# Optimization experiments

Hardware: AMD Instinct MI355X
Metric: run time of the kernel (lower is better)

## Reference

```python
import jax, jax.numpy as jnp
import numpy as np
from jax import lax

B, VLEN, H, DIM, C = 32, 2048, 1024, 1024, 32  # batch, value len, hidden_dim, dim, conv_out_channel


def setup_inputs() -> dict:
    key = jax.random.key(0)
    ks = jax.random.split(key, 13)
    s = 0.02
    return {
        "query": jax.random.normal(ks[0], (B, 1, H), dtype=jnp.float32),
        "value": jax.random.normal(ks[1], (B, VLEN, H), dtype=jnp.float32),
        "prev_attn": jax.random.uniform(ks[2], (B, VLEN), dtype=jnp.float32),
        "conv_w": jax.random.normal(ks[3], (C, 1, 3), dtype=jnp.float32) * s,   # Conv1d weight (out,in,k)
        "conv_b": jax.random.normal(ks[4], (C,), dtype=jnp.float32) * s,
        "w_loc": jax.random.normal(ks[5], (DIM, C), dtype=jnp.float32) * s,     # loc_projection (no bias)
        "w_q": jax.random.normal(ks[6], (DIM, H), dtype=jnp.float32) * s,       # query_projection (no bias)
        "w_v": jax.random.normal(ks[7], (DIM, H), dtype=jnp.float32) * s,       # value_projection (no bias)
        "bias": jax.random.uniform(ks[8], (DIM,), dtype=jnp.float32, minval=-0.1, maxval=0.1),
        "w_score": jax.random.normal(ks[9], (1, DIM), dtype=jnp.float32) * s,   # score_projection weight
        "b_score": jax.random.normal(ks[10], (1,), dtype=jnp.float32) * s,
        "w_out": jax.random.normal(ks[11], (H, 2 * H), dtype=jnp.float32) * s,  # out_projection weight
        "b_out": jax.random.normal(ks[12], (H,), dtype=jnp.float32) * s,
    }


def reference(query, value, prev_attn, conv_w, conv_b, w_loc, w_q, w_v, bias,
              w_score, b_score, w_out, b_out):
    # Location features: Conv1d(1 -> C, k=3, pad=1) over prev_attn, then transpose to (B, V, C)
    conv = lax.conv_general_dilated(
        prev_attn[:, None, :], conv_w, window_strides=(1,), padding=[(1, 1)],
        dimension_numbers=("NCH", "OIH", "NCH"),
    ) + conv_b[None, :, None]                       # (B, C, V)
    conv_feat = jnp.transpose(conv, (0, 2, 1))      # (B, V, C)

    qp = jnp.einsum("bqh,dh->bqd", query, w_q)      # (B, 1, DIM)
    vp = jnp.einsum("bvh,dh->bvd", value, w_v)      # (B, V, DIM)
    lp = jnp.einsum("bvc,dc->bvd", conv_feat, w_loc)

    e = jnp.tanh(qp + vp + lp + bias)               # (B, V, DIM), qp broadcasts over V
    score = jnp.einsum("bvd,d->bv", e, w_score[0]) + b_score[0]  # (B, V)

    # smoothing=True: sigmoid then normalize
    s = jax.nn.sigmoid(score)
    attn = s / jnp.sum(s, axis=-1, keepdims=True)   # (B, V)

    context = jnp.einsum("bv,bvh->bh", attn, value)               # (B, H)
    combined = jnp.concatenate([context[:, None, :], query], axis=2)  # (B, 1, 2H)
    output = jnp.einsum("bqk,hk->bqh", combined, w_out) + b_out       # (B, 1, H)
    return output, attn
```

## Files before the change

### kernel.cpp

```cpp
#include <hip/hip_runtime.h>
#include <hip/hip_bf16.h>
#include <math.h>

#define B_SZ 32
#define VLEN_SZ 2048
#define H_SZ 1024
#define DIM_SZ 1024
#define C_SZ 32

typedef float f32x4 __attribute__((ext_vector_type(4)));
typedef short s16x8 __attribute__((ext_vector_type(8)));
typedef short s16x4 __attribute__((ext_vector_type(4)));
typedef unsigned int u32x4 __attribute__((ext_vector_type(4)));

__device__ __forceinline__ short f2bf(float f) {
  unsigned u = __float_as_uint(f);
  u = (u + 0x7fffu + ((u >> 16) & 1u)) >> 16;
  return (short)u;
}

__device__ __forceinline__ float bf2f(short s) {
  return __uint_as_float(((unsigned)(unsigned short)s) << 16);
}

__device__ __forceinline__ unsigned pack2(float a, float b) {
  return __builtin_amdgcn_perm(__float_as_uint(b), __float_as_uint(a), 0x07060302u);
}

__device__ __forceinline__ float fast_tanh(float x) {
  float z = __expf(2.0f * x);
  return 1.0f - 2.0f / (z + 1.0f);
}

__device__ __forceinline__ void ldg_lds16(const void* g, void* l) {
  __builtin_amdgcn_global_load_lds(
      (const __attribute__((address_space(1))) unsigned int*)g,
      (__attribute__((address_space(3))) unsigned int*)l, 16, 0, 0);
}

__global__ __launch_bounds__(256) void k_prep(
    const float* __restrict__ query, const float* __restrict__ w_q,
    const float* __restrict__ bias, const float* __restrict__ prev,
    const float* __restrict__ conv_w, const float* __restrict__ conv_b,
    const float* __restrict__ w_loc, const float* __restrict__ w_v,
    const float* __restrict__ value,
    float* __restrict__ qpb, short* __restrict__ cfb, short* __restrict__ wlocb,
    short* __restrict__ wvb, short* __restrict__ vb,
    float* __restrict__ score, float* __restrict__ context) {
  int bid = blockIdx.x;
  int t = threadIdx.x;
  if (bid < 8192) {
    int wid = bid * 4 + (t >> 6);
    int lane = t & 63;
    int d = wid >> 5;
    int b = wid & 31;
    const f32x4* q4 = (const f32x4*)(query + (size_t)b * H_SZ);
    const f32x4* w4 = (const f32x4*)(w_q + (size_t)d * H_SZ);
    float acc = 0.f;
#pragma unroll
    for (int it = 0; it < 4; ++it) {
      int k = it * 64 + lane;
      f32x4 a = q4[k], w = w4[k];
      acc += a[0] * w[0] + a[1] * w[1] + a[2] * w[2] + a[3] * w[3];
    }
#pragma unroll
    for (int off = 32; off; off >>= 1) acc += __shfl_xor(acc, off, 64);
    if (lane == 0) qpb[(size_t)b * DIM_SZ + d] = acc + bias[d];
  } else if (bid < 8448) {
    int r = (bid - 8192) * 256 + t;
    int v = r & (VLEN_SZ - 1);
    float p0 = prev[r];
    float pm = (v > 0) ? prev[r - 1] : 0.f;
    float pp = (v < VLEN_SZ - 1) ? prev[r + 1] : 0.f;
    float o[C_SZ];
#pragma unroll
    for (int c = 0; c < C_SZ; ++c)
      o[c] = conv_b[c] + pm * conv_w[c * 3 + 0] + p0 * conv_w[c * 3 + 1] + pp * conv_w[c * 3 + 2];
    s16x8* dst = (s16x8*)(cfb + (size_t)r * C_SZ);
#pragma unroll
    for (int g = 0; g < 4; ++g) {
      s16x8 pk;
#pragma unroll
      for (int e = 0; e < 8; ++e) pk[e] = f2bf(o[8 * g + e]);
      dst[g] = pk;
    }
  } else if (bid < 8480) {
    int i = (bid - 8448) * 256 + t;
    f32x4 v = ((const f32x4*)w_loc)[i];
    s16x4 o;
    o[0] = f2bf(v[0]); o[1] = f2bf(v[1]); o[2] = f2bf(v[2]); o[3] = f2bf(v[3]);
    ((s16x4*)wlocb)[i] = o;
  } else if (bid < 9504) {
    int i = (bid - 8480) * 256 + t;
    f32x4 v = ((const f32x4*)w_v)[i];
    s16x4 o;
    o[0] = f2bf(v[0]); o[1] = f2bf(v[1]); o[2] = f2bf(v[2]); o[3] = f2bf(v[3]);
    ((s16x4*)wvb)[i] = o;
  } else if (bid < 9568) {
    int i = (bid - 9504) * 256 + t;
    ((f32x4*)score)[i] = (f32x4){0.f, 0.f, 0.f, 0.f};
  } else if (bid < 9600) {
    int i = (bid - 9568) * 256 + t;
    ((f32x4*)context)[i] = (f32x4){0.f, 0.f, 0.f, 0.f};
  } else {
    size_t i = (size_t)(bid - 9600) * 256 + t;
    const f32x4* src = (const f32x4*)value;
    f32x4 v0 = src[2 * i], v1 = src[2 * i + 1];
    s16x8 o;
    o[0] = f2bf(v0[0]); o[1] = f2bf(v0[1]); o[2] = f2bf(v0[2]); o[3] = f2bf(v0[3]);
    o[4] = f2bf(v1[0]); o[5] = f2bf(v1[1]); o[6] = f2bf(v1[2]); o[7] = f2bf(v1[3]);
    ((s16x8*)vb)[i] = o;
  }
}

#define STAGE_A(ktv, bi_)                                                    \
  do {                                                                       \
    const short* s0_ = ((ktv) < 32) ? aBaseV + (size_t)(ktv) * 32 : aBaseC;  \
    const short* s1_ = ((ktv) < 32) ? aBaseV + (size_t)(ktv) * 32 + 131072   \
                                    : aBaseC + 4096;                         \
    ldg_lds16(s0_, ldw + (bi_) * 16384);                                     \
    ldg_lds16(s1_, ldw + (bi_) * 16384 + 4096);                              \
  } while (0)

#define STAGE_B(ktv, bi_)                                                    \
  do {                                                                       \
    const short* s0_ = ((ktv) < 32) ? bBaseV + (size_t)(ktv) * 32 : bBaseC;  \
    const short* s1_ = ((ktv) < 32) ? bBaseV + (size_t)(ktv) * 32 + 131072   \
                                    : bBaseC + 4096;                         \
    ldg_lds16(s0_, ldw + (bi_) * 16384 + 8192);                              \
    ldg_lds16(s1_, ldw + (bi_) * 16384 + 12288);                             \
  } while (0)

__global__ __launch_bounds__(512, 2) void k_score8(
    const short* __restrict__ vb, const short* __restrict__ wvb,
    const short* __restrict__ wlocb, const short* __restrict__ cfb,
    const float* __restrict__ qpb, const float* __restrict__ w_score,
    float* __restrict__ score) {
  __shared__ short lds_s[3 * 16384];
  __shared__ float sred[8][128];

  int t = threadIdx.x;
  int w = t >> 6, l = t & 63;
  int q = l >> 4, l16 = l & 15;
  int wm = w >> 2, wn = w & 3;
  int bid = blockIdx.x;
  int x = bid & 7, j = bid >> 3;
  int nt = j & 3, mt = x * 32 + (j >> 2);
  int row0 = mt * 256, d0 = nt * 256;
  int b = row0 >> 11;

  int ar = l >> 2;
  int cc = ((l & 3) ^ ((l >> 3) & 3)) * 8;
  int roff = w * 16 + ar;
  const short* aBaseV = vb + (size_t)(row0 + roff) * H_SZ + cc;
  const short* bBaseV = wvb + (size_t)(d0 + roff) * H_SZ + cc;
  const short* aBaseC = cfb + (size_t)(row0 + roff) * C_SZ + cc;
  const short* bBaseC = wlocb + (size_t)(d0 + roff) * C_SZ + cc;
  short* ldw = lds_s + w * 512;

  int posf = (q ^ ((l16 >> 1) & 3)) * 8;

  f32x4 acc[8][4];
#pragma unroll
  for (int i = 0; i < 8; ++i)
#pragma unroll
    for (int n = 0; n < 4; ++n) acc[i][n] = (f32x4){0.f, 0.f, 0.f, 0.f};

  STAGE_A(0, 0); STAGE_B(0, 0);
  STAGE_A(1, 1); STAGE_B(1, 1);
  asm volatile("s_waitcnt vmcnt(4)" ::: "memory");
  __builtin_amdgcn_s_barrier();

  int bi = 0, bs = 2;
  for (int kt = 0; kt < 33; ++kt) {
    const short* As = lds_s + bi * 16384;
    const short* Bs = As + 8192;
    if (kt <= 30) { STAGE_A(kt + 2, bs); STAGE_B(kt + 2, bs); }

    s16x8 af[8], bf[4];
#pragma unroll
    for (int m = 0; m < 8; ++m)
      af[m] = *(const s16x8*)(As + (wm * 128 + m * 16 + l16) * 32 + posf);
#pragma unroll
    for (int n = 0; n < 4; ++n)
      bf[n] = *(const s16x8*)(Bs + (wn * 64 + n * 16 + l16) * 32 + posf);

    __builtin_amdgcn_s_setprio(1);
#pragma unroll
    for (int m = 0; m < 8; ++m)
#pragma unroll
      for (int n = 0; n < 4; ++n)
        acc[m][n] = __builtin_amdgcn_mfma_f32_16x16x32_bf16(af[m], bf[n], acc[m][n], 0, 0, 0);
    __builtin_amdgcn_s_setprio(0);

    if (kt < 31) {
      asm volatile("s_waitcnt vmcnt(4)" ::: "memory");
    } else if (kt == 31) {
      asm volatile("s_waitcnt vmcnt(0)" ::: "memory");
    }
    __builtin_amdgcn_s_barrier();
    bi = (bi == 2) ? 0 : bi + 1;
    bs = (bs == 2) ? 0 : bs + 1;
  }

  float qv[4], wv[4];
#pragma unroll
  for (int n = 0; n < 4; ++n) {
    int d = d0 + wn * 64 + n * 16 + l16;
    qv[n] = qpb[(size_t)b * DIM_SZ + d];
    wv[n] = w_score[d];
  }
#pragma unroll
  for (int i = 0; i < 8; ++i) {
#pragma unroll
    for (int r = 0; r < 4; ++r) {
      float part = 0.f;
#pragma unroll
      for (int n = 0; n < 4; ++n)
        part += fast_tanh(acc[i][n][r] + qv[n]) * wv[n];
      part += __shfl_xor(part, 1);
      part += __shfl_xor(part, 2);
      part += __shfl_xor(part, 4);
      part += __shfl_xor(part, 8);
      if (l16 == 0) sred[w][i * 16 + q * 4 + r] = part;
    }
  }
  __syncthreads();
  if (t < 256) {
    int wmh = t >> 7, lr = t & 127;
    float v = sred[wmh * 4][lr] + sred[wmh * 4 + 1][lr] +
              sred[wmh * 4 + 2][lr] + sred[wmh * 4 + 3][lr];
    atomicAdd(&score[row0 + t], v);
  }
}

__global__ __launch_bounds__(256) void k_prep_f32(
    const float* __restrict__ query, const float* __restrict__ w_q,
    const float* __restrict__ bias, const float* __restrict__ prev,
    const float* __restrict__ conv_w, const float* __restrict__ conv_b,
    const float* __restrict__ w_loc, const float* __restrict__ w_v,
    float* __restrict__ qpb, float* __restrict__ cff, short* __restrict__ wlocb,
    short* __restrict__ wvb, float* __restrict__ score, float* __restrict__ context) {
  int bid = blockIdx.x;
  int t = threadIdx.x;
  if (bid < 8192) {
    int wid = bid * 4 + (t >> 6);
    int lane = t & 63;
    int d = wid >> 5;
    int b = wid & 31;
    const f32x4* q4 = (const f32x4*)(query + (size_t)b * H_SZ);
    const f32x4* w4 = (const f32x4*)(w_q + (size_t)d * H_SZ);
    float acc = 0.f;
#pragma unroll
    for (int it = 0; it < 4; ++it) {
      int k = it * 64 + lane;
      f32x4 a = q4[k], w = w4[k];
      acc += a[0] * w[0] + a[1] * w[1] + a[2] * w[2] + a[3] * w[3];
    }
#pragma unroll
    for (int off = 32; off; off >>= 1) acc += __shfl_xor(acc, off, 64);
    if (lane == 0) qpb[(size_t)b * DIM_SZ + d] = acc + bias[d];
  } else if (bid < 8448) {
    int r = (bid - 8192) * 256 + t;
    int v = r & (VLEN_SZ - 1);
    float p0 = prev[r];
    float pm = (v > 0) ? prev[r - 1] : 0.f;
    float pp = (v < VLEN_SZ - 1) ? prev[r + 1] : 0.f;
    float o[C_SZ];
#pragma unroll
    for (int c = 0; c < C_SZ; ++c)
      o[c] = conv_b[c] + pm * conv_w[c * 3 + 0] + p0 * conv_w[c * 3 + 1] + pp * conv_w[c * 3 + 2];
    f32x4* dst = (f32x4*)(cff + (size_t)r * C_SZ);
#pragma unroll
    for (int g = 0; g < 8; ++g)
      dst[g] = (f32x4){o[4 * g], o[4 * g + 1], o[4 * g + 2], o[4 * g + 3]};
  } else if (bid < 8480) {
    int i = (bid - 8448) * 256 + t;
    f32x4 v = ((const f32x4*)w_loc)[i];
    s16x4 o;
    o[0] = f2bf(v[0]); o[1] = f2bf(v[1]); o[2] = f2bf(v[2]); o[3] = f2bf(v[3]);
    ((s16x4*)wlocb)[i] = o;
  } else if (bid < 9504) {
    int i = (bid - 8480) * 256 + t;
    f32x4 v = ((const f32x4*)w_v)[i];
    s16x4 o;
    o[0] = f2bf(v[0]); o[1] = f2bf(v[1]); o[2] = f2bf(v[2]); o[3] = f2bf(v[3]);
    ((s16x4*)wvb)[i] = o;
  } else if (bid < 9568) {
    int i = (bid - 9504) * 256 + t;
    ((f32x4*)score)[i] = (f32x4){0.f, 0.f, 0.f, 0.f};
  } else {
    int i = (bid - 9568) * 256 + t;
    ((f32x4*)context)[i] = (f32x4){0.f, 0.f, 0.f, 0.f};
  }
}

__global__ __launch_bounds__(256, 4) void k_score_f32(
    const float* __restrict__ value, const short* __restrict__ wvb,
    const short* __restrict__ wlocb, const float* __restrict__ cff,
    const float* __restrict__ qpb, const float* __restrict__ w_score,
    float* __restrict__ score) {
  __shared__ float As[128 * 32];
  __shared__ short Bs[128 * 32];
  __shared__ float sred[4][64];

  int t = threadIdx.x;
  int w = t >> 6, l = t & 63;
  int q = l >> 4, l16 = l & 15;
  int bid = blockIdx.x;
  int x = bid & 7;
  int j = bid >> 3;
  int nt = j & 7;
  int mt = x * 64 + (j >> 3);
  int row0 = mt * 128;
  int d0 = nt * 128;
  int b = row0 >> 11;
  int wm = w >> 1, wn = w & 1;

  int ar = l >> 3;
  int ac = (l & 7) ^ ar;
  const float* gA[4];
  float* lA[4];
#pragma unroll
  for (int s = 0; s < 4; ++s) {
    gA[s] = value + (size_t)(row0 + 32 * w + 8 * s + ar) * H_SZ + ac * 4;
    lA[s] = As + (32 * w + 8 * s) * 32;
  }
  int lr = l >> 2;
  int kc = ((l & 3) ^ ((l >> 3) & 3)) * 8;
  const short* gB0 = wvb + (size_t)(d0 + 32 * w + lr) * H_SZ + kc;
  const short* gB1 = wvb + (size_t)(d0 + 32 * w + 16 + lr) * H_SZ + kc;
  short* lB0 = Bs + (32 * w) * 32;
  short* lB1 = Bs + (32 * w + 16) * 32;

  int h7 = l16 & 7;
  int pA0 = ((2 * q) ^ h7) * 4;
  int pA1 = ((2 * q + 1) ^ h7) * 4;
  int posB = (q ^ ((l16 >> 1) & 3)) * 8;

  f32x4 acc[4][4];
#pragma unroll
  for (int i = 0; i < 4; ++i)
#pragma unroll
    for (int jj = 0; jj < 4; ++jj) acc[i][jj] = (f32x4){0.f, 0.f, 0.f, 0.f};

  for (int kt = 0; kt <= 32; ++kt) {
    if (kt < 32) {
      int k0 = kt * 32;
#pragma unroll
      for (int s = 0; s < 4; ++s) ldg_lds16(gA[s] + k0, lA[s]);
      ldg_lds16(gB0 + (size_t)k0, lB0);
      ldg_lds16(gB1 + (size_t)k0, lB1);
    } else {
#pragma unroll
      for (int s = 0; s < 4; ++s)
        ldg_lds16(cff + (size_t)(row0 + 32 * w + 8 * s + ar) * C_SZ + ac * 4, lA[s]);
      ldg_lds16(wlocb + (size_t)(d0 + 32 * w + lr) * C_SZ + kc, lB0);
      ldg_lds16(wlocb + (size_t)(d0 + 32 * w + 16 + lr) * C_SZ + kc, lB1);
    }
    __syncthreads();

    s16x8 a[4], bb[4];
#pragma unroll
    for (int i = 0; i < 4; ++i) {
      const float* rowp = As + (wm * 64 + i * 16 + l16) * 32;
      f32x4 f0 = *(const f32x4*)(rowp + pA0);
      f32x4 f1 = *(const f32x4*)(rowp + pA1);
      u32x4 pk;
      pk[0] = pack2(f0[0], f0[1]);
      pk[1] = pack2(f0[2], f0[3]);
      pk[2] = pack2(f1[0], f1[1]);
      pk[3] = pack2(f1[2], f1[3]);
      a[i] = *(s16x8*)&pk;
    }
#pragma unroll
    for (int jj = 0; jj < 4; ++jj)
      bb[jj] = *(const s16x8*)(Bs + (wn * 64 + jj * 16 + l16) * 32 + posB);
#pragma unroll
    for (int i = 0; i < 4; ++i)
#pragma unroll
      for (int jj = 0; jj < 4; ++jj)
        acc[i][jj] = __builtin_amdgcn_mfma_f32_16x16x32_bf16(a[i], bb[jj], acc[i][jj], 0, 0, 0);
    __syncthreads();
  }

  float qv[4], wv[4];
#pragma unroll
  for (int jj = 0; jj < 4; ++jj) {
    int d = d0 + wn * 64 + jj * 16 + l16;
    qv[jj] = qpb[(size_t)b * DIM_SZ + d];
    wv[jj] = w_score[d];
  }

#pragma unroll
  for (int i = 0; i < 4; ++i) {
#pragma unroll
    for (int r = 0; r < 4; ++r) {
      float part = 0.f;
#pragma unroll
      for (int jj = 0; jj < 4; ++jj)
        part += fast_tanh(acc[i][jj][r] + qv[jj]) * wv[jj];
      part += __shfl_xor(part, 1);
      part += __shfl_xor(part, 2);
      part += __shfl_xor(part, 4);
      part += __shfl_xor(part, 8);
      if (l16 == 0) sred[w][i * 16 + q * 4 + r] = part;
    }
  }
  __syncthreads();
  if (t < 128) {
    int half = t >> 6;
    float v = sred[half * 2][t & 63] + sred[half * 2 + 1][t & 63];
    atomicAdd(&score[row0 + t], v);
  }
}

__global__ __launch_bounds__(256) void k_ctx(
    const float* __restrict__ score, const float* __restrict__ b_score,
    const short* __restrict__ vb, float* __restrict__ attn_out,
    float* __restrict__ context) {
  __shared__ float als[VLEN_SZ];
  __shared__ float red[4];
  int b = blockIdx.x, vc = blockIdx.y, t = threadIdx.x;
  float bs = b_score[0];
  float sv[8];
  float lsum = 0.f;
  int v0 = t * 8;
#pragma unroll
  for (int k = 0; k < 8; ++k) {
    float ps = score[(size_t)b * VLEN_SZ + v0 + k] + bs;
    float s = 1.0f / (1.0f + __expf(-ps));
    sv[k] = s;
    lsum += s;
    als[v0 + k] = s;
  }
#pragma unroll
  for (int off = 32; off; off >>= 1) lsum += __shfl_xor(lsum, off, 64);
  if ((t & 63) == 0) red[t >> 6] = lsum;
  __syncthreads();
  float inv = 1.0f / (red[0] + red[1] + red[2] + red[3]);
  if (vc == 0) {
#pragma unroll
    for (int k = 0; k < 8; ++k)
      attn_out[(size_t)b * VLEN_SZ + v0 + k] = sv[k] * inv;
  }

  int h0 = t * 4;
  int vbase = vc * 128;
  const short* vp = vb + ((size_t)b * VLEN_SZ + vbase) * H_SZ + h0;
  const float* av = als + vbase;
  f32x4 acc = (f32x4){0.f, 0.f, 0.f, 0.f};
#pragma unroll 8
  for (int v = 0; v < 128; ++v) {
    s16x4 xv = *(const s16x4*)(vp + (size_t)v * H_SZ);
    float a = av[v];
    acc[0] += a * bf2f(xv[0]); acc[1] += a * bf2f(xv[1]);
    acc[2] += a * bf2f(xv[2]); acc[3] += a * bf2f(xv[3]);
  }
#pragma unroll
  for (int k = 0; k < 4; ++k)
    atomicAdd(&context[(size_t)b * H_SZ + h0 + k], acc[k] * inv);
}

__global__ __launch_bounds__(256) void k_ctx_f32(
    const float* __restrict__ score, const float* __restrict__ b_score,
    const float* __restrict__ value, float* __restrict__ attn_out,
    float* __restrict__ context) {
  __shared__ float als[VLEN_SZ];
  __shared__ float red[4];
  int b = blockIdx.x, vc = blockIdx.y, t = threadIdx.x;
  float bs = b_score[0];
  float sv[8];
  float lsum = 0.f;
  int v0 = t * 8;
#pragma unroll
  for (int k = 0; k < 8; ++k) {
    float ps = score[(size_t)b * VLEN_SZ + v0 + k] + bs;
    float s = 1.0f / (1.0f + __expf(-ps));
    sv[k] = s;
    lsum += s;
    als[v0 + k] = s;
  }
#pragma unroll
  for (int off = 32; off; off >>= 1) lsum += __shfl_xor(lsum, off, 64);
  if ((t & 63) == 0) red[t >> 6] = lsum;
  __syncthreads();
  float inv = 1.0f / (red[0] + red[1] + red[2] + red[3]);
  if (vc == 0) {
#pragma unroll
    for (int k = 0; k < 8; ++k)
      attn_out[(size_t)b * VLEN_SZ + v0 + k] = sv[k] * inv;
  }

  int h0 = t * 4;
  int vbase = vc * 128;
  const float* vp = value + ((size_t)b * VLEN_SZ + vbase) * H_SZ + h0;
  const float* av = als + vbase;
  f32x4 acc = (f32x4){0.f, 0.f, 0.f, 0.f};
#pragma unroll 8
  for (int v = 0; v < 128; ++v) {
    f32x4 xv = *(const f32x4*)(vp + (size_t)v * H_SZ);
    float a = av[v];
    acc[0] += a * xv[0]; acc[1] += a * xv[1];
    acc[2] += a * xv[2]; acc[3] += a * xv[3];
  }
#pragma unroll
  for (int k = 0; k < 4; ++k)
    atomicAdd(&context[(size_t)b * H_SZ + h0 + k], acc[k] * inv);
}

__global__ void k_out(const float* __restrict__ context, const float* __restrict__ query,
                      const float* __restrict__ w_out, const float* __restrict__ b_out,
                      float* __restrict__ out) {
  int wid = blockIdx.x * 4 + (threadIdx.x >> 6);
  int lane = threadIdx.x & 63;
  int h = wid >> 5;
  int b = wid & 31;
  const f32x4* w4 = (const f32x4*)(w_out + (size_t)h * 2048);
  const f32x4* c4 = (const f32x4*)(context + (size_t)b * H_SZ);
  const f32x4* q4 = (const f32x4*)(query + (size_t)b * H_SZ);
  float acc = 0.f;
#pragma unroll
  for (int it = 0; it < 8; ++it) {
    int k4 = it * 64 + lane;
    f32x4 w = w4[k4];
    f32x4 c = (k4 < 256) ? c4[k4] : q4[k4 - 256];
    acc += w[0] * c[0] + w[1] * c[1] + w[2] * c[2] + w[3] * c[3];
  }
#pragma unroll
  for (int off = 32; off; off >>= 1) acc += __shfl_xor(acc, off, 64);
  if (lane == 0) out[(size_t)b * H_SZ + h] = acc + b_out[h];
}

extern "C" void kernel_launch(void* const* d_in, const int* in_sizes, int n_in,
                              void* d_out, int out_size, void* d_ws, size_t ws_size,
                              hipStream_t stream) {
  const float* query   = (const float*)d_in[0];
  const float* value   = (const float*)d_in[1];
  const float* prev    = (const float*)d_in[2];
  const float* conv_w  = (const float*)d_in[3];
  const float* conv_b  = (const float*)d_in[4];
  const float* w_loc   = (const float*)d_in[5];
  const float* w_q     = (const float*)d_in[6];
  const float* w_v     = (const float*)d_in[7];
  const float* bias    = (const float*)d_in[8];
  const float* w_score = (const float*)d_in[9];
  const float* b_score = (const float*)d_in[10];
  const float* w_out   = (const float*)d_in[11];
  const float* b_out   = (const float*)d_in[12];

  float* out  = (float*)d_out;
  float* attn = out + B_SZ * H_SZ;

  char* ws = (char*)d_ws;
  float* score   = (float*)(ws);
  float* qpb     = (float*)(ws + (256 << 10));
  float* context = (float*)(ws + (384 << 10));
  short* wvb     = (short*)(ws + (512 << 10));
  short* wlocb   = (short*)(ws + (2560 << 10));

  size_t need = ((size_t)16 << 20) + ((size_t)128 << 20);
  if (ws_size >= need) {
    short* cfb = (short*)(ws + (3 << 20));
    short* vb  = (short*)(ws + ((size_t)16 << 20));
    k_prep<<<42368, 256, 0, stream>>>(query, w_q, bias, prev, conv_w, conv_b,
                                      w_loc, w_v, value, qpb, cfb, wlocb, wvb, vb,
                                      score, context);
    k_score8<<<1024, 512, 0, stream>>>(vb, wvb, wlocb, cfb, qpb, w_score, score);
    k_ctx<<<dim3(B_SZ, 16), 256, 0, stream>>>(score, b_score, vb, attn, context);
  } else {
    float* cff = (float*)(ws + (3 << 20));
    k_prep_f32<<<9600, 256, 0, stream>>>(query, w_q, bias, prev, conv_w, conv_b,
                                         w_loc, w_v, qpb, cff, wlocb, wvb, score, context);
    k_score_f32<<<4096, 256, 0, stream>>>(value, wvb, wlocb, cff, qpb, w_score, score);
    k_ctx_f32<<<dim3(B_SZ, 16), 256, 0, stream>>>(score, b_score, value, attn, context);
  }
  k_out<<<(B_SZ * H_SZ) / 4, 256, 0, stream>>>(context, query, w_out, b_out, out);
}
```

Before: 677.2 us.

## Replace 256x256 triple-buffered score GEMM with 128x128 32x32x16 MFMA kernel

The main score GEMM moves from a 256x256 tile, 512-thread, triple-buffered kernel using 16x16x32 MFMA to a 128x128 tile, 256-thread kernel using 32x32x16 MFMA. The new kernel uses a simpler single-buffer LDS layout with two syncthreads per K step. Separately, the query projection in the prep kernel now has each wave keep its w_q row in registers and loop over the batch, cutting prep blocks from 8192 to 256. The trade-off is that smaller tiles double global traffic per FLOP and remove the software prefetch pipeline, in exchange for higher occupancy and more blocks.

New measurement: 715.2 us. 1.06x slower.

```diff
diff --git a/kernel.cpp b/kernel.cpp
--- a/kernel.cpp
+++ b/kernel.cpp
@@ -9,6 +9,7 @@
 #define C_SZ 32
 
 typedef float f32x4 __attribute__((ext_vector_type(4)));
+typedef float f32x16 __attribute__((ext_vector_type(16)));
 typedef short s16x8 __attribute__((ext_vector_type(8)));
 typedef short s16x4 __attribute__((ext_vector_type(4)));
 typedef unsigned int u32x4 __attribute__((ext_vector_type(4)));
@@ -49,25 +50,28 @@
     float* __restrict__ score, float* __restrict__ context) {
   int bid = blockIdx.x;
   int t = threadIdx.x;
-  if (bid < 8192) {
-    int wid = bid * 4 + (t >> 6);
-    int lane = t & 63;
-    int d = wid >> 5;
-    int b = wid & 31;
-    const f32x4* q4 = (const f32x4*)(query + (size_t)b * H_SZ);
+  if (bid < 256) {
+    int d = bid * 4 + (t >> 6);
+    int l = t & 63;
     const f32x4* w4 = (const f32x4*)(w_q + (size_t)d * H_SZ);
-    float acc = 0.f;
-#pragma unroll
-    for (int it = 0; it < 4; ++it) {
-      int k = it * 64 + lane;
-      f32x4 a = q4[k], w = w4[k];
-      acc += a[0] * w[0] + a[1] * w[1] + a[2] * w[2] + a[3] * w[3];
-    }
-#pragma unroll
-    for (int off = 32; off; off >>= 1) acc += __shfl_xor(acc, off, 64);
-    if (lane == 0) qpb[(size_t)b * DIM_SZ + d] = acc + bias[d];
-  } else if (bid < 8448) {
-    int r = (bid - 8192) * 256 + t;
+    f32x4 wq[4];
+#pragma unroll
+    for (int it = 0; it < 4; ++it) wq[it] = w4[it * 64 + l];
+    float bd = bias[d];
+    for (int b = 0; b < B_SZ; ++b) {
+      const f32x4* q4 = (const f32x4*)(query + (size_t)b * H_SZ);
+      float acc = 0.f;
+#pragma unroll
+      for (int it = 0; it < 4; ++it) {
+        f32x4 a = q4[it * 64 + l];
+        acc += a[0] * wq[it][0] + a[1] * wq[it][1] + a[2] * wq[it][2] + a[3] * wq[it][3];
+      }
+#pragma unroll
+      for (int off = 32; off; off >>= 1) acc += __shfl_xor(acc, off, 64);
+      if (l == 0) qpb[(size_t)b * DIM_SZ + d] = acc + bd;
+    }
+  } else if (bid < 512) {
+    int r = (bid - 256) * 256 + t;
     int v = r & (VLEN_SZ - 1);
     float p0 = prev[r];
     float pm = (v > 0) ? prev[r - 1] : 0.f;
@@ -84,26 +88,26 @@
       for (int e = 0; e < 8; ++e) pk[e] = f2bf(o[8 * g + e]);
       dst[g] = pk;
     }
-  } else if (bid < 8480) {
-    int i = (bid - 8448) * 256 + t;
+  } else if (bid < 544) {
+    int i = (bid - 512) * 256 + t;
     f32x4 v = ((const f32x4*)w_loc)[i];
     s16x4 o;
     o[0] = f2bf(v[0]); o[1] = f2bf(v[1]); o[2] = f2bf(v[2]); o[3] = f2bf(v[3]);
     ((s16x4*)wlocb)[i] = o;
-  } else if (bid < 9504) {
-    int i = (bid - 8480) * 256 + t;
+  } else if (bid < 1568) {
+    int i = (bid - 544) * 256 + t;
     f32x4 v = ((const f32x4*)w_v)[i];
     s16x4 o;
     o[0] = f2bf(v[0]); o[1] = f2bf(v[1]); o[2] = f2bf(v[2]); o[3] = f2bf(v[3]);
     ((s16x4*)wvb)[i] = o;
-  } else if (bid < 9568) {
-    int i = (bid - 9504) * 256 + t;
+  } else if (bid < 1632) {
+    int i = (bid - 1568) * 256 + t;
     ((f32x4*)score)[i] = (f32x4){0.f, 0.f, 0.f, 0.f};
-  } else if (bid < 9600) {
-    int i = (bid - 9568) * 256 + t;
+  } else if (bid < 1664) {
+    int i = (bid - 1632) * 256 + t;
     ((f32x4*)context)[i] = (f32x4){0.f, 0.f, 0.f, 0.f};
   } else {
-    size_t i = (size_t)(bid - 9600) * 256 + t;
+    size_t i = (size_t)(bid - 1664) * 256 + t;
     const f32x4* src = (const f32x4*)value;
     f32x4 v0 = src[2 * i], v1 = src[2 * i + 1];
     s16x8 o;
@@ -113,123 +117,111 @@
   }
 }
 
-#define STAGE_A(ktv, bi_)                                                    \
-  do {                                                                       \
-    const short* s0_ = ((ktv) < 32) ? aBaseV + (size_t)(ktv) * 32 : aBaseC;  \
-    const short* s1_ = ((ktv) < 32) ? aBaseV + (size_t)(ktv) * 32 + 131072   \
-                                    : aBaseC + 4096;                         \
-    ldg_lds16(s0_, ldw + (bi_) * 16384);                                     \
-    ldg_lds16(s1_, ldw + (bi_) * 16384 + 4096);                              \
-  } while (0)
-
-#define STAGE_B(ktv, bi_)                                                    \
-  do {                                                                       \
-    const short* s0_ = ((ktv) < 32) ? bBaseV + (size_t)(ktv) * 32 : bBaseC;  \
-    const short* s1_ = ((ktv) < 32) ? bBaseV + (size_t)(ktv) * 32 + 131072   \
-                                    : bBaseC + 4096;                         \
-    ldg_lds16(s0_, ldw + (bi_) * 16384 + 8192);                              \
-    ldg_lds16(s1_, ldw + (bi_) * 16384 + 12288);                             \
-  } while (0)
-
-__global__ __launch_bounds__(512, 2) void k_score8(
+__global__ __launch_bounds__(256, 4) void k_score32(
     const short* __restrict__ vb, const short* __restrict__ wvb,
     const short* __restrict__ wlocb, const short* __restrict__ cfb,
     const float* __restrict__ qpb, const float* __restrict__ w_score,
     float* __restrict__ score) {
-  __shared__ short lds_s[3 * 16384];
-  __shared__ float sred[8][128];
+  __shared__ short As[4096];
+  __shared__ short Bs[4096];
+  __shared__ float sred[4][64];
 
   int t = threadIdx.x;
   int w = t >> 6, l = t & 63;
-  int q = l >> 4, l16 = l & 15;
-  int wm = w >> 2, wn = w & 3;
+  int l32 = l & 31, hi = l >> 5;
   int bid = blockIdx.x;
-  int x = bid & 7, j = bid >> 3;
-  int nt = j & 3, mt = x * 32 + (j >> 2);
-  int row0 = mt * 256, d0 = nt * 256;
+  int x = bid & 7;
+  int j = bid >> 3;
+  int nt = j & 7;
+  int mt = x * 64 + (j >> 3);
+  int row0 = mt * 128;
+  int d0 = nt * 128;
   int b = row0 >> 11;
-
-  int ar = l >> 2;
-  int cc = ((l & 3) ^ ((l >> 3) & 3)) * 8;
-  int roff = w * 16 + ar;
-  const short* aBaseV = vb + (size_t)(row0 + roff) * H_SZ + cc;
-  const short* bBaseV = wvb + (size_t)(d0 + roff) * H_SZ + cc;
-  const short* aBaseC = cfb + (size_t)(row0 + roff) * C_SZ + cc;
-  const short* bBaseC = wlocb + (size_t)(d0 + roff) * C_SZ + cc;
-  short* ldw = lds_s + w * 512;
-
-  int posf = (q ^ ((l16 >> 1) & 3)) * 8;
-
-  f32x4 acc[8][4];
-#pragma unroll
-  for (int i = 0; i < 8; ++i)
-#pragma unroll
-    for (int n = 0; n < 4; ++n) acc[i][n] = (f32x4){0.f, 0.f, 0.f, 0.f};
-
-  STAGE_A(0, 0); STAGE_B(0, 0);
-  STAGE_A(1, 1); STAGE_B(1, 1);
-  asm volatile("s_waitcnt vmcnt(4)" ::: "memory");
-  __builtin_amdgcn_s_barrier();
-
-  int bi = 0, bs = 2;
-  for (int kt = 0; kt < 33; ++kt) {
-    const short* As = lds_s + bi * 16384;
-    const short* Bs = As + 8192;
-    if (kt <= 30) { STAGE_A(kt + 2, bs); STAGE_B(kt + 2, bs); }
-
-    s16x8 af[8], bf[4];
-#pragma unroll
-    for (int m = 0; m < 8; ++m)
-      af[m] = *(const s16x8*)(As + (wm * 128 + m * 16 + l16) * 32 + posf);
-#pragma unroll
-    for (int n = 0; n < 4; ++n)
-      bf[n] = *(const s16x8*)(Bs + (wn * 64 + n * 16 + l16) * 32 + posf);
-
-    __builtin_amdgcn_s_setprio(1);
-#pragma unroll
-    for (int m = 0; m < 8; ++m)
-#pragma unroll
-      for (int n = 0; n < 4; ++n)
-        acc[m][n] = __builtin_amdgcn_mfma_f32_16x16x32_bf16(af[m], bf[n], acc[m][n], 0, 0, 0);
-    __builtin_amdgcn_s_setprio(0);
-
-    if (kt < 31) {
-      asm volatile("s_waitcnt vmcnt(4)" ::: "memory");
-    } else if (kt == 31) {
-      asm volatile("s_waitcnt vmcnt(0)" ::: "memory");
-    }
-    __builtin_amdgcn_s_barrier();
-    bi = (bi == 2) ? 0 : bi + 1;
-    bs = (bs == 2) ? 0 : bs + 1;
-  }
-
-  float qv[4], wv[4];
-#pragma unroll
-  for (int n = 0; n < 4; ++n) {
-    int d = d0 + wn * 64 + n * 16 + l16;
-    qv[n] = qpb[(size_t)b * DIM_SZ + d];
-    wv[n] = w_score[d];
-  }
-#pragma unroll
-  for (int i = 0; i < 8; ++i) {
-#pragma unroll
-    for (int r = 0; r < 4; ++r) {
-      float part = 0.f;
-#pragma unroll
-      for (int n = 0; n < 4; ++n)
-        part += fast_tanh(acc[i][n][r] + qv[n]) * wv[n];
+  int wm = w >> 1, wn = w & 1;
+
+  const short* gA = vb + (size_t)(row0 + l) * H_SZ + w * 8;
+  const short* gB = wvb + (size_t)(d0 + l) * H_SZ + w * 8;
+  const short* gAc = cfb + (size_t)(row0 + l) * C_SZ + w * 8;
+  const short* gBc = wlocb + (size_t)(d0 + l) * C_SZ + w * 8;
+  short* lA0 = As + (w * 128) * 8;
+  short* lA1 = As + (w * 128 + 64) * 8;
+  short* lB0 = Bs + (w * 128) * 8;
+  short* lB1 = Bs + (w * 128 + 64) * 8;
+  size_t rstep = (size_t)64 * H_SZ;
+  size_t rstepc = (size_t)64 * C_SZ;
+
+  f32x16 acc[2][2];
+#pragma unroll
+  for (int mi = 0; mi < 2; ++mi)
+#pragma unroll
+    for (int nj = 0; nj < 2; ++nj)
+#pragma unroll
+      for (int r = 0; r < 16; ++r) acc[mi][nj][r] = 0.f;
+
+  for (int kt = 0; kt <= 32; ++kt) {
+    if (kt < 32) {
+      size_t k0 = (size_t)kt * 32;
+      ldg_lds16(gA + k0, lA0);
+      ldg_lds16(gA + k0 + rstep, lA1);
+      ldg_lds16(gB + k0, lB0);
+      ldg_lds16(gB + k0 + rstep, lB1);
+    } else {
+      ldg_lds16(gAc, lA0);
+      ldg_lds16(gAc + rstepc, lA1);
+      ldg_lds16(gBc, lB0);
+      ldg_lds16(gBc + rstepc, lB1);
+    }
+    __syncthreads();
+
+    s16x8 af[2][2], bf[2][2];
+#pragma unroll
+    for (int mi = 0; mi < 2; ++mi)
+#pragma unroll
+      for (int ks = 0; ks < 2; ++ks) {
+        int c = ks * 2 + hi;
+        af[mi][ks] = *(const s16x8*)(As + (c * 128 + wm * 64 + mi * 32 + l32) * 8);
+        bf[mi][ks] = *(const s16x8*)(Bs + (c * 128 + wn * 64 + mi * 32 + l32) * 8);
+      }
+#pragma unroll
+    for (int ks = 0; ks < 2; ++ks)
+#pragma unroll
+      for (int mi = 0; mi < 2; ++mi)
+#pragma unroll
+        for (int nj = 0; nj < 2; ++nj)
+          acc[mi][nj] = __builtin_amdgcn_mfma_f32_32x32x16_bf16(
+              af[mi][ks], bf[nj][ks], acc[mi][nj], 0, 0, 0);
+    __syncthreads();
+  }
+
+  float qv[2], wv[2];
+#pragma unroll
+  for (int nj = 0; nj < 2; ++nj) {
+    int d = d0 + wn * 64 + nj * 32 + l32;
+    qv[nj] = qpb[(size_t)b * DIM_SZ + d];
+    wv[nj] = w_score[d];
+  }
+
+#pragma unroll
+  for (int mi = 0; mi < 2; ++mi) {
+#pragma unroll
+    for (int r = 0; r < 16; ++r) {
+      float part = fast_tanh(acc[mi][0][r] + qv[0]) * wv[0] +
+                   fast_tanh(acc[mi][1][r] + qv[1]) * wv[1];
       part += __shfl_xor(part, 1);
       part += __shfl_xor(part, 2);
       part += __shfl_xor(part, 4);
       part += __shfl_xor(part, 8);
-      if (l16 == 0) sred[w][i * 16 + q * 4 + r] = part;
+      part += __shfl_xor(part, 16);
+      if (l32 == 0) {
+        int rowin = mi * 32 + (r & 3) + 8 * (r >> 2) + 4 * hi;
+        sred[w][rowin] = part;
+      }
     }
   }
   __syncthreads();
-  if (t < 256) {
-    int wmh = t >> 7, lr = t & 127;
-    float v = sred[wmh * 4][lr] + sred[wmh * 4 + 1][lr] +
-              sred[wmh * 4 + 2][lr] + sred[wmh * 4 + 3][lr];
+  if (t < 128) {
+    int half = t >> 6;
+    float v = sred[half * 2][t & 63] + sred[half * 2 + 1][t & 63];
     atomicAdd(&score[row0 + t], v);
   }
 }
@@ -300,8 +292,8 @@
     const short* __restrict__ wlocb, const float* __restrict__ cff,
     const float* __restrict__ qpb, const float* __restrict__ w_score,
     float* __restrict__ score) {
-  __shared__ float As[128 * 32];
-  __shared__ short Bs[128 * 32];
+  __shared__ float Asf[128 * 32];
+  __shared__ short Bsf[128 * 32];
   __shared__ float sred[4][64];
 
   int t = threadIdx.x;
@@ -324,14 +316,14 @@
 #pragma unroll
   for (int s = 0; s < 4; ++s) {
     gA[s] = value + (size_t)(row0 + 32 * w + 8 * s + ar) * H_SZ + ac * 4;
-    lA[s] = As + (32 * w + 8 * s) * 32;
+    lA[s] = Asf + (32 * w + 8 * s) * 32;
   }
   int lr = l >> 2;
   int kc = ((l & 3) ^ ((l >> 3) & 3)) * 8;
   const short* gB0 = wvb + (size_t)(d0 + 32 * w + lr) * H_SZ + kc;
   const short* gB1 = wvb + (size_t)(d0 + 32 * w + 16 + lr) * H_SZ + kc;
-  short* lB0 = Bs + (32 * w) * 32;
-  short* lB1 = Bs + (32 * w + 16) * 32;
+  short* lB0 = Bsf + (32 * w) * 32;
+  short* lB1 = Bsf + (32 * w + 16) * 32;
 
   int h7 = l16 & 7;
   int pA0 = ((2 * q) ^ h7) * 4;
@@ -363,7 +355,7 @@
     s16x8 a[4], bb[4];
 #pragma unroll
     for (int i = 0; i < 4; ++i) {
-      const float* rowp = As + (wm * 64 + i * 16 + l16) * 32;
+      const float* rowp = Asf + (wm * 64 + i * 16 + l16) * 32;
       f32x4 f0 = *(const f32x4*)(rowp + pA0);
       f32x4 f1 = *(const f32x4*)(rowp + pA1);
       u32x4 pk;
@@ -375,7 +367,7 @@
     }
 #pragma unroll
     for (int jj = 0; jj < 4; ++jj)
-      bb[jj] = *(const s16x8*)(Bs + (wn * 64 + jj * 16 + l16) * 32 + posB);
+      bb[jj] = *(const s16x8*)(Bsf + (wn * 64 + jj * 16 + l16) * 32 + posB);
 #pragma unroll
     for (int i = 0; i < 4; ++i)
 #pragma unroll
@@ -563,10 +555,10 @@
   if (ws_size >= need) {
     short* cfb = (short*)(ws + (3 << 20));
     short* vb  = (short*)(ws + ((size_t)16 << 20));
-    k_prep<<<42368, 256, 0, stream>>>(query, w_q, bias, prev, conv_w, conv_b,
+    k_prep<<<34432, 256, 0, stream>>>(query, w_q, bias, prev, conv_w, conv_b,
                                       w_loc, w_v, value, qpb, cfb, wlocb, wvb, vb,
                                       score, context);
-    k_score8<<<1024, 512, 0, stream>>>(vb, wvb, wlocb, cfb, qpb, w_score, score);
+    k_score32<<<4096, 256, 0, stream>>>(vb, wvb, wlocb, cfb, qpb, w_score, score);
     k_ctx<<<dim3(B_SZ, 16), 256, 0, stream>>>(score, b_score, vb, attn, context);
   } else {
     float* cff = (float*)(ws + (3 << 20));
```
